# Kernel tuning notes

Hardware: AMD Instinct MI355X
Metric: run time of the kernel (lower is better)

## Reference

```python
import jax, jax.numpy as jnp
import numpy as np

N = 8192
E = 262144
H = 64


def setup_inputs() -> dict:
    key = jax.random.key(0)
    ks = jax.random.split(key, 9)
    edge_index = jax.random.randint(ks[0], (2, E), 0, N, dtype=jnp.int64)
    edge_attr = jax.random.uniform(ks[1], (E,), dtype=jnp.float32)
    node_features = jax.random.normal(ks[2], (N, N), dtype=jnp.float32)
    # GCNConv weights (glorot-ish scale) and biases
    W1 = jax.random.normal(ks[3], (N, H), dtype=jnp.float32) / np.sqrt(N)
    b1 = jnp.zeros((H,), dtype=jnp.float32)
    W2 = jax.random.normal(ks[4], (H, H), dtype=jnp.float32) / np.sqrt(H)
    b2 = jnp.zeros((H,), dtype=jnp.float32)
    fcW = jax.random.normal(ks[5], (H, N), dtype=jnp.float32) / np.sqrt(H)
    fcb = jnp.zeros((N,), dtype=jnp.float32)
    return {"edge_index": edge_index, "edge_attr": edge_attr,
            "node_features": node_features,
            "W1": W1, "b1": b1, "W2": W2, "b2": b2,
            "fcW": fcW, "fcb": fcb}


def _gcn_conv(x, W, b, src, dst, ew, n_nodes):
    # PyG GCNConv with edge weights: x' = D^{-1/2} (A + I) D^{-1/2} (x W) + b
    # src/dst/ew already include self-loops (weight 1.0).
    x = x @ W                                        # [N, out]
    deg = jax.ops.segment_sum(ew, dst, num_segments=n_nodes)  # in-degree w/ loops
    dinv = jax.lax.rsqrt(deg)                        # deg >= 1 due to self loops
    norm = dinv[src] * ew * dinv[dst]                # [E+N]
    out = jax.ops.segment_sum(x[src] * norm[:, None], dst, num_segments=n_nodes)
    return out + b


def reference(edge_index, edge_attr, node_features, W1, b1, W2, b2, fcW, fcb):
    n_nodes = node_features.shape[0]
    loops = jnp.arange(n_nodes, dtype=edge_index.dtype)
    src = jnp.concatenate([edge_index[0], loops])
    dst = jnp.concatenate([edge_index[1], loops])
    ew = jnp.concatenate([edge_attr, jnp.ones((n_nodes,), edge_attr.dtype)])
    x = jax.nn.relu(_gcn_conv(node_features, W1, b1, src, dst, ew, n_nodes))
    x = jax.nn.relu(_gcn_conv(x, W2, b2, src, dst, ew, n_nodes))
    x = x @ fcW + fcb
    return jax.nn.softmax(x, axis=-1)
```

## Files before the change

### kernel.cpp

```cpp
#include <hip/hip_runtime.h>


#define NN 8192
#define NE 262144
#define HD 64
#define KCH 1024
#define NKC 8

typedef float f32x4 __attribute__((ext_vector_type(4)));
typedef short v8s   __attribute__((ext_vector_type(8)));
typedef unsigned short ushort_t;

__device__ __forceinline__ unsigned short bf16_rne(float f){
  union { float f; unsigned u; } v; v.f = f;
  unsigned r = v.u + 0x7fffu + ((v.u >> 16) & 1u);
  return (unsigned short)(r >> 16);
}
__device__ __forceinline__ float bf16_f32(unsigned short h){
  union { unsigned u; float f; } v; v.u = ((unsigned)h) << 16;
  return v.f;
}
__device__ __forceinline__ f32x4 mfma16(v8s a, v8s b, f32x4 c){
  return __builtin_amdgcn_mfma_f32_16x16x32_bf16(a, b, c, 0, 0, 0);
}

__global__ void k_prep0(const float* __restrict__ W1, const float* __restrict__ fcW,
                        ushort_t* w1hi, ushort_t* w1lo, ushort_t* fcwp,
                        float* deg, int* cnt, int* wcnt, float* S){
  int idx = blockIdx.x*blockDim.x + threadIdx.x;
  if (idx < NN){ deg[idx]=1.0f; cnt[idx]=0; wcnt[idx]=0; S[idx]=0.0f; }
  {
    int kk = idx & 31, c = (idx>>5)&15, nt = (idx>>9)&3, kb = idx>>11;
    int k = kb*32 + kk, col = nt*16 + c;
    float w = W1[(size_t)k*HD + col];
    unsigned short hi = bf16_rne(w);
    w1hi[idx] = hi;
    w1lo[idx] = bf16_rne(w - bf16_f32(hi));
  }
  {
    int kk = idx & 31, c = (idx>>5)&15, cblk = (idx>>9)&511, kb = idx>>18;
    int k = kb*32 + kk, col = cblk*16 + c;
    fcwp[idx] = bf16_rne(fcW[(size_t)k*NN + col]);
  }
}

__global__ void k_deg_cnt(const int* ei, const float* ew, float* deg, int* cnt){
  int e = blockIdx.x*blockDim.x + threadIdx.x;
  if (e < NE){
    int d = ei[NE + e];
    atomicAdd(&deg[d], ew[e]);
    atomicAdd(&cnt[d], 1);
  }
}

__global__ void k_scan(const int* cnt, const float* deg, int* rowptr, float* dinv){
  __shared__ int part[256];
  int t = threadIdx.x;
  int loc[32]; int s = 0;
  #pragma unroll
  for (int j=0;j<32;++j){ loc[j] = cnt[t*32+j]; s += loc[j]; }
  part[t] = s; __syncthreads();
  for (int off=1; off<256; off<<=1){
    int v = (t >= off) ? part[t-off] : 0;
    __syncthreads();
    part[t] += v;
    __syncthreads();
  }
  int run = part[t] - s;
  #pragma unroll
  for (int j=0;j<32;++j){ rowptr[t*32+j] = run; run += loc[j]; }
  if (t == 255) rowptr[NN] = run;
  #pragma unroll
  for (int j=0;j<32;++j) dinv[t*32+j] = 1.0f / sqrtf(deg[t*32+j]);
}

__global__ void k_fill(const int* ei, const float* ew, const float* dinv,
                       const int* rowptr, int* wcnt, int* csr_src, float* csr_nrm){
  int e = blockIdx.x*blockDim.x + threadIdx.x;
  if (e < NE){
    int s = ei[e], d = ei[NE+e];
    int slot = rowptr[d] + atomicAdd(&wcnt[d], 1);
    csr_src[slot] = s;
    csr_nrm[slot] = dinv[s] * ew[e] * dinv[d];
  }
}

__global__ __launch_bounds__(256) void k_gemm1(const float* __restrict__ X,
                                               const ushort_t* __restrict__ w1hi,
                                               const ushort_t* __restrict__ w1lo,
                                               float* __restrict__ xw1p){
  int lane = threadIdx.x & 63, w = threadIdx.x >> 6;
  int r = lane & 15, seg = lane >> 4;
  int row = blockIdx.x*64 + w*16 + r;
  int kb0 = blockIdx.y * KCH;
  const float* xr = X + (size_t)row * NN + kb0 + seg*8;

  f32x4 z = {0.f,0.f,0.f,0.f};
  f32x4 acc[4] = {z,z,z,z};

  f32x4 p0 = *(const f32x4*)(xr);
  f32x4 p1 = *(const f32x4*)(xr + 4);

  for (int it = 0; it < KCH/32; ++it){
    f32x4 c0 = p0, c1 = p1;
    if (it < KCH/32 - 1){
      p0 = *(const f32x4*)(xr + (it+1)*32);
      p1 = *(const f32x4*)(xr + (it+1)*32 + 4);
    }
    v8s ah, al;
    #pragma unroll
    for (int j=0;j<4;++j){
      float f = c0[j]; unsigned short h = bf16_rne(f);
      ah[j] = (short)h; al[j] = (short)bf16_rne(f - bf16_f32(h));
      f = c1[j]; h = bf16_rne(f);
      ah[4+j] = (short)h; al[4+j] = (short)bf16_rne(f - bf16_f32(h));
    }
    int kbb = (kb0 >> 5) + it;
    #pragma unroll
    for (int nt=0; nt<4; ++nt){
      size_t boff = ((size_t)(kbb*4 + nt)*16 + r)*32 + seg*8;
      v8s bh = *(const v8s*)(w1hi + boff);
      v8s bl = *(const v8s*)(w1lo + boff);
      acc[nt] = mfma16(ah, bh, acc[nt]);
      acc[nt] = mfma16(ah, bl, acc[nt]);
      acc[nt] = mfma16(al, bh, acc[nt]);
    }
  }

  float* o = xw1p + (size_t)blockIdx.y*(NN*HD) + (size_t)(blockIdx.x*64 + w*16)*HD;
  #pragma unroll
  for (int nt=0; nt<4; ++nt)
    #pragma unroll
    for (int j=0;j<4;++j)
      o[(4*seg + j)*HD + nt*16 + r] = acc[nt][j];
}

__global__ __launch_bounds__(256) void k_red(const float* __restrict__ xw1p,
                                             float* __restrict__ xw1){
  int i = blockIdx.x*blockDim.x + threadIdx.x;
  f32x4 s = {0.f,0.f,0.f,0.f};
  #pragma unroll
  for (int c=0;c<NKC;++c){
    f32x4 v = *(const f32x4*)(xw1p + (size_t)c*NN*HD + (size_t)i*4);
    s[0]+=v[0]; s[1]+=v[1]; s[2]+=v[2]; s[3]+=v[3];
  }
  *(f32x4*)(xw1 + (size_t)i*4) = s;
}

__global__ __launch_bounds__(256) void k_agg1c(const float* __restrict__ xin,
                                               const float* __restrict__ b1,
                                               const float* __restrict__ W2,
                                               const float* __restrict__ dinv,
                                               const int* __restrict__ rowptr,
                                               const int* __restrict__ csr_src,
                                               const float* __restrict__ csr_nrm,
                                               float* __restrict__ x2w){
  __shared__ float W2s[64*64];
  __shared__ float rows[4][64];
  int lane = threadIdx.x & 63, w = threadIdx.x >> 6;
  for (int o = threadIdx.x; o < 64*64; o += 256) W2s[o] = W2[o];
  __syncthreads();

  int i = blockIdx.x*4 + w;
  float di = dinv[i];
  float acc = di*di * xin[(size_t)i*HD + lane];
  int e = rowptr[i], e1 = rowptr[i+1];
  for (; e + 1 < e1; e += 2){
    int s0 = csr_src[e], s1 = csr_src[e+1];
    float n0 = csr_nrm[e], n1 = csr_nrm[e+1];
    acc += n0 * xin[(size_t)s0*HD + lane];
    acc += n1 * xin[(size_t)s1*HD + lane];
  }
  if (e < e1) acc += csr_nrm[e] * xin[(size_t)csr_src[e]*HD + lane];
  float v = acc + b1[lane];
  rows[w][lane] = v > 0.f ? v : 0.f;
  __syncthreads();

  float acc2 = 0.f;
  #pragma unroll
  for (int k=0;k<64;++k) acc2 += rows[w][k] * W2s[k*64 + lane];
  x2w[(size_t)i*HD + lane] = acc2;
}

__global__ __launch_bounds__(256) void k_agg2(const float* __restrict__ xin,
                                              const float* __restrict__ b2,
                                              const float* __restrict__ dinv,
                                              const int* __restrict__ rowptr,
                                              const int* __restrict__ csr_src,
                                              const float* __restrict__ csr_nrm,
                                              ushort_t* __restrict__ x2b){
  int lane = threadIdx.x & 63, w = threadIdx.x >> 6;
  int i = blockIdx.x*4 + w;
  float di = dinv[i];
  float acc = di*di * xin[(size_t)i*HD + lane];
  int e = rowptr[i], e1 = rowptr[i+1];
  for (; e + 1 < e1; e += 2){
    int s0 = csr_src[e], s1 = csr_src[e+1];
    float n0 = csr_nrm[e], n1 = csr_nrm[e+1];
    acc += n0 * xin[(size_t)s0*HD + lane];
    acc += n1 * xin[(size_t)s1*HD + lane];
  }
  if (e < e1) acc += csr_nrm[e] * xin[(size_t)csr_src[e]*HD + lane];
  float v = acc + b2[lane];
  v = v > 0.f ? v : 0.f;
  x2b[(size_t)i*HD + lane] = bf16_rne(v);
}

__global__ __launch_bounds__(256) void k_rowsum(const ushort_t* __restrict__ x2b,
                                                const ushort_t* __restrict__ fcwp,
                                                const float* __restrict__ fcb,
                                                float* __restrict__ S){
  int lane = threadIdx.x & 63, w = threadIdx.x >> 6;
  int r = lane & 15, seg = lane >> 4;
  int row0 = blockIdx.x*128 + w*32;
  const ushort_t* xb = x2b + (size_t)(row0 + r)*HD + seg*8;
  v8s x00 = *(const v8s*)(xb);
  v8s x01 = *(const v8s*)(xb + 32);
  v8s x10 = *(const v8s*)(xb + 16*HD);
  v8s x11 = *(const v8s*)(xb + 16*HD + 32);
  float rp0 = 0.f, rp1 = 0.f;
  for (int cb=0; cb<4; ++cb){
    int colbase = blockIdx.y*256 + cb*64;
    f32x4 z = {0.f,0.f,0.f,0.f};
    f32x4 acc0[4] = {z,z,z,z}, acc1[4] = {z,z,z,z};
    #pragma unroll
    for (int nt=0; nt<4; ++nt){
      int cblk = (colbase >> 4) + nt;
      v8s bA = *(const v8s*)(fcwp + ((size_t)cblk*16 + r)*32 + seg*8);
      v8s bB = *(const v8s*)(fcwp + ((size_t)(512 + cblk)*16 + r)*32 + seg*8);
      acc0[nt] = mfma16(bA, x00, acc0[nt]);
      acc0[nt] = mfma16(bB, x01, acc0[nt]);
      acc1[nt] = mfma16(bA, x10, acc1[nt]);
      acc1[nt] = mfma16(bB, x11, acc1[nt]);
    }
    #pragma unroll
    for (int nt=0; nt<4; ++nt){
      int col = colbase + nt*16 + seg*4;
      f32x4 fb = *(const f32x4*)(fcb + col);
      #pragma unroll
      for (int j=0;j<4;++j){
        rp0 += __expf(acc0[nt][j] + fb[j]);
        rp1 += __expf(acc1[nt][j] + fb[j]);
      }
    }
  }
  rp0 += __shfl_xor(rp0, 16); rp0 += __shfl_xor(rp0, 32);
  rp1 += __shfl_xor(rp1, 16); rp1 += __shfl_xor(rp1, 32);
  if (lane < 16){
    atomicAdd(&S[row0 + lane],      rp0);
    atomicAdd(&S[row0 + 16 + lane], rp1);
  }
}

__global__ __launch_bounds__(256) void k_passB(const ushort_t* __restrict__ x2b,
                                               const ushort_t* __restrict__ fcwp,
                                               const float* __restrict__ fcb,
                                               const float* __restrict__ S,
                                               float* __restrict__ out){
  int lane = threadIdx.x & 63, w = threadIdx.x >> 6;
  int r = lane & 15, seg = lane >> 4;
  int row0 = blockIdx.x*128 + w*32;
  const ushort_t* xb = x2b + (size_t)(row0 + r)*HD + seg*8;
  v8s x00 = *(const v8s*)(xb);
  v8s x01 = *(const v8s*)(xb + 32);
  v8s x10 = *(const v8s*)(xb + 16*HD);
  v8s x11 = *(const v8s*)(xb + 16*HD + 32);
  float si0 = 1.0f / S[row0 + r];
  float si1 = 1.0f / S[row0 + 16 + r];
  float* o0 = out + (size_t)(row0 + r)*NN;
  float* o1 = out + (size_t)(row0 + 16 + r)*NN;
  for (int cb=0; cb<4; ++cb){
    int colbase = blockIdx.y*256 + cb*64;
    f32x4 z = {0.f,0.f,0.f,0.f};
    f32x4 acc0[4] = {z,z,z,z}, acc1[4] = {z,z,z,z};
    #pragma unroll
    for (int nt=0; nt<4; ++nt){
      int cblk = (colbase >> 4) + nt;
      v8s bA = *(const v8s*)(fcwp + ((size_t)cblk*16 + r)*32 + seg*8);
      v8s bB = *(const v8s*)(fcwp + ((size_t)(512 + cblk)*16 + r)*32 + seg*8);
      acc0[nt] = mfma16(bA, x00, acc0[nt]);
      acc0[nt] = mfma16(bB, x01, acc0[nt]);
      acc1[nt] = mfma16(bA, x10, acc1[nt]);
      acc1[nt] = mfma16(bB, x11, acc1[nt]);
    }
    #pragma unroll
    for (int nt=0; nt<4; ++nt){
      int col = colbase + nt*16 + seg*4;
      f32x4 fb = *(const f32x4*)(fcb + col);
      f32x4 v0, v1;
      #pragma unroll
      for (int j=0;j<4;++j){
        v0[j] = __expf(acc0[nt][j] + fb[j]) * si0;
        v1[j] = __expf(acc1[nt][j] + fb[j]) * si1;
      }
      *(f32x4*)(o0 + col) = v0;
      *(f32x4*)(o1 + col) = v1;
    }
  }
}

extern "C" void kernel_launch(void* const* d_in, const int* in_sizes, int n_in,
                              void* d_out, int out_size, void* d_ws, size_t ws_size,
                              hipStream_t stream){
  (void)in_sizes; (void)n_in; (void)out_size; (void)ws_size;
  const int*   ei  = (const int*)  d_in[0];
  const float* ew  = (const float*)d_in[1];
  const float* X   = (const float*)d_in[2];
  const float* W1  = (const float*)d_in[3];
  const float* b1  = (const float*)d_in[4];
  const float* W2  = (const float*)d_in[5];
  const float* b2  = (const float*)d_in[6];
  const float* fcW = (const float*)d_in[7];
  const float* fcb = (const float*)d_in[8];
  float* out = (float*)d_out;
  char*  ws  = (char*)d_ws;

  float*    deg     = (float*)   (ws + 0);
  float*    dinv    = (float*)   (ws + 32768);
  int*      cnt     = (int*)     (ws + 65536);
  int*      wcnt    = (int*)     (ws + 98304);
  int*      rowptr  = (int*)     (ws + 131072);
  int*      csr_src = (int*)     (ws + 167936);
  float*    csr_nrm = (float*)   (ws + 1216512);
  ushort_t* w1hi    = (ushort_t*)(ws + 2265088);
  ushort_t* w1lo    = (ushort_t*)(ws + 3313664);
  ushort_t* fcwp    = (ushort_t*)(ws + 4362240);
  float*    xw1p    = (float*)   (ws + 5410816);
  float*    xw1     = (float*)   (ws + 22188032);
  float*    x2w     = (float*)   (ws + 24285184);
  ushort_t* x2b     = (ushort_t*)(ws + 26382336);
  float*    S       = (float*)   (ws + 27430912);

  k_prep0   <<<2048, 256, 0, stream>>>(W1, fcW, w1hi, w1lo, fcwp, deg, cnt, wcnt, S);
  k_deg_cnt <<<1024, 256, 0, stream>>>(ei, ew, deg, cnt);
  k_scan    <<<1,    256, 0, stream>>>(cnt, deg, rowptr, dinv);
  k_fill    <<<1024, 256, 0, stream>>>(ei, ew, dinv, rowptr, wcnt, csr_src, csr_nrm);
  k_gemm1   <<<dim3(128, NKC), 256, 0, stream>>>(X, w1hi, w1lo, xw1p);
  k_red     <<<512,  256, 0, stream>>>(xw1p, xw1);
  k_agg1c   <<<2048, 256, 0, stream>>>(xw1, b1, W2, dinv, rowptr, csr_src, csr_nrm, x2w);
  k_agg2    <<<2048, 256, 0, stream>>>(x2w, b2, dinv, rowptr, csr_src, csr_nrm, x2b);
  k_rowsum  <<<dim3(64,32), 256, 0, stream>>>(x2b, fcwp, fcb, S);
  k_passB   <<<dim3(64,32), 256, 0, stream>>>(x2b, fcwp, fcb, S, out);
}
```

Baseline: 320.8 us.

## Register-block two row tiles per wave in GEMM1 with double-buffered prefetch

Each wave in the split-bf16 GEMM over X·W1 now computes 32 rows instead of 16, so every W1 hi/lo fragment loaded feeds twice as many MFMAs and the grid halves. A and B fragments are double-buffered two iterations ahead in registers, and the fp32-to-bf16 hi/lo split uses truncation instead of round-to-nearest-even to save ALU work. In exchange the kernel holds more registers, which launch_bounds(256,2) tries to bound, and the grid drops to 512 blocks, which may leave CUs underused. Truncation also changes the rounding of the hi/lo split slightly.

```diff
diff --git a/kernel.cpp b/kernel.cpp
--- a/kernel.cpp
+++ b/kernel.cpp
@@ -22,6 +22,14 @@
 }
 __device__ __forceinline__ f32x4 mfma16(v8s a, v8s b, f32x4 c){
   return __builtin_amdgcn_mfma_f32_16x16x32_bf16(a, b, c, 0, 0, 0);
+}
+
+__device__ __forceinline__ void split_tr(float f, short& hi, short& lo){
+  unsigned u = __float_as_uint(f);
+  hi = (short)(u >> 16);
+  float fh = __uint_as_float(u & 0xffff0000u);
+  float d = f - fh;
+  lo = (short)(__float_as_uint(d) >> 16);
 }
 
 __global__ void k_prep0(const float* __restrict__ W1, const float* __restrict__ fcW,
@@ -85,54 +93,82 @@
   }
 }
 
-__global__ __launch_bounds__(256) void k_gemm1(const float* __restrict__ X,
-                                               const ushort_t* __restrict__ w1hi,
-                                               const ushort_t* __restrict__ w1lo,
-                                               float* __restrict__ xw1p){
+__global__ __launch_bounds__(256, 2) void k_gemm1(const float* __restrict__ X,
+                                                  const ushort_t* __restrict__ w1hi,
+                                                  const ushort_t* __restrict__ w1lo,
+                                                  float* __restrict__ xw1p){
   int lane = threadIdx.x & 63, w = threadIdx.x >> 6;
   int r = lane & 15, seg = lane >> 4;
-  int row = blockIdx.x*64 + w*16 + r;
+  int row0 = blockIdx.x*128 + w*32;
   int kb0 = blockIdx.y * KCH;
-  const float* xr = X + (size_t)row * NN + kb0 + seg*8;
+  const float* xr0 = X + (size_t)(row0 + r)      * NN + kb0 + seg*8;
+  const float* xr1 = X + (size_t)(row0 + 16 + r) * NN + kb0 + seg*8;
+  const ushort_t* bhp = w1hi + (size_t)(kb0 >> 5)*2048 + r*32 + seg*8;
+  const ushort_t* blp = w1lo + (size_t)(kb0 >> 5)*2048 + r*32 + seg*8;
 
   f32x4 z = {0.f,0.f,0.f,0.f};
-  f32x4 acc[4] = {z,z,z,z};
-
-  f32x4 p0 = *(const f32x4*)(xr);
-  f32x4 p1 = *(const f32x4*)(xr + 4);
-
-  for (int it = 0; it < KCH/32; ++it){
-    f32x4 c0 = p0, c1 = p1;
-    if (it < KCH/32 - 1){
-      p0 = *(const f32x4*)(xr + (it+1)*32);
-      p1 = *(const f32x4*)(xr + (it+1)*32 + 4);
-    }
-    v8s ah, al;
+  f32x4 acc0[4] = {z,z,z,z};
+  f32x4 acc1[4] = {z,z,z,z};
+
+  f32x4 A00_0, A01_0, A10_0, A11_0;
+  f32x4 A00_1, A01_1, A10_1, A11_1;
+  v8s bh0[4], bl0[4], bh1[4], bl1[4];
+
+  A00_0 = *(const f32x4*)(xr0);        A01_0 = *(const f32x4*)(xr0 + 4);
+  A10_0 = *(const f32x4*)(xr1);        A11_0 = *(const f32x4*)(xr1 + 4);
+  A00_1 = *(const f32x4*)(xr0 + 32);   A01_1 = *(const f32x4*)(xr0 + 36);
+  A10_1 = *(const f32x4*)(xr1 + 32);   A11_1 = *(const f32x4*)(xr1 + 36);
+  #pragma unroll
+  for (int nt=0; nt<4; ++nt){
+    bh0[nt] = *(const v8s*)(bhp + nt*512);
+    bl0[nt] = *(const v8s*)(blp + nt*512);
+    bh1[nt] = *(const v8s*)(bhp + 2048 + nt*512);
+    bl1[nt] = *(const v8s*)(blp + 2048 + nt*512);
+  }
+
+  auto body = [&](int it, f32x4& A00, f32x4& A01, f32x4& A10, f32x4& A11,
+                  v8s (&bh)[4], v8s (&bl)[4]){
+    v8s ah0, al0, ah1, al1;
     #pragma unroll
     for (int j=0;j<4;++j){
-      float f = c0[j]; unsigned short h = bf16_rne(f);
-      ah[j] = (short)h; al[j] = (short)bf16_rne(f - bf16_f32(h));
-      f = c1[j]; h = bf16_rne(f);
-      ah[4+j] = (short)h; al[4+j] = (short)bf16_rne(f - bf16_f32(h));
-    }
-    int kbb = (kb0 >> 5) + it;
-    #pragma unroll
-    for (int nt=0; nt<4; ++nt){
-      size_t boff = ((size_t)(kbb*4 + nt)*16 + r)*32 + seg*8;
-      v8s bh = *(const v8s*)(w1hi + boff);
-      v8s bl = *(const v8s*)(w1lo + boff);
-      acc[nt] = mfma16(ah, bh, acc[nt]);
-      acc[nt] = mfma16(ah, bl, acc[nt]);
-      acc[nt] = mfma16(al, bh, acc[nt]);
-    }
-  }
-
-  float* o = xw1p + (size_t)blockIdx.y*(NN*HD) + (size_t)(blockIdx.x*64 + w*16)*HD;
+      short h,l;
+      split_tr(A00[j], h, l); ah0[j]   = h; al0[j]   = l;
+      split_tr(A01[j], h, l); ah0[4+j] = h; al0[4+j] = l;
+      split_tr(A10[j], h, l); ah1[j]   = h; al1[j]   = l;
+      split_tr(A11[j], h, l); ah1[4+j] = h; al1[4+j] = l;
+    }
+    int itn = (it + 2) & 31;
+    A00 = *(const f32x4*)(xr0 + itn*32);  A01 = *(const f32x4*)(xr0 + itn*32 + 4);
+    A10 = *(const f32x4*)(xr1 + itn*32);  A11 = *(const f32x4*)(xr1 + itn*32 + 4);
+    #pragma unroll
+    for (int nt=0; nt<4; ++nt){
+      acc0[nt] = mfma16(ah0, bh[nt], acc0[nt]);
+      acc0[nt] = mfma16(ah0, bl[nt], acc0[nt]);
+      acc0[nt] = mfma16(al0, bh[nt], acc0[nt]);
+      acc1[nt] = mfma16(ah1, bh[nt], acc1[nt]);
+      acc1[nt] = mfma16(ah1, bl[nt], acc1[nt]);
+      acc1[nt] = mfma16(al1, bh[nt], acc1[nt]);
+    }
+    #pragma unroll
+    for (int nt=0; nt<4; ++nt){
+      bh[nt] = *(const v8s*)(bhp + (size_t)itn*2048 + nt*512);
+      bl[nt] = *(const v8s*)(blp + (size_t)itn*2048 + nt*512);
+    }
+  };
+
+  for (int j = 0; j < 16; ++j){
+    body(2*j,     A00_0, A01_0, A10_0, A11_0, bh0, bl0);
+    body(2*j + 1, A00_1, A01_1, A10_1, A11_1, bh1, bl1);
+  }
+
+  float* o = xw1p + (size_t)blockIdx.y*(NN*HD) + (size_t)row0*HD;
   #pragma unroll
   for (int nt=0; nt<4; ++nt)
     #pragma unroll
-    for (int j=0;j<4;++j)
-      o[(4*seg + j)*HD + nt*16 + r] = acc[nt][j];
+    for (int j=0;j<4;++j){
+      o[(4*seg + j)*HD + nt*16 + r]        = acc0[nt][j];
+      o[(16 + 4*seg + j)*HD + nt*16 + r]   = acc1[nt][j];
+    }
 }
 
 __global__ __launch_bounds__(256) void k_red(const float* __restrict__ xw1p,
@@ -335,7 +371,7 @@
   k_deg_cnt <<<1024, 256, 0, stream>>>(ei, ew, deg, cnt);
   k_scan    <<<1,    256, 0, stream>>>(cnt, deg, rowptr, dinv);
   k_fill    <<<1024, 256, 0, stream>>>(ei, ew, dinv, rowptr, wcnt, csr_src, csr_nrm);
-  k_gemm1   <<<dim3(128, NKC), 256, 0, stream>>>(X, w1hi, w1lo, xw1p);
+  k_gemm1   <<<dim3(64, NKC), 256, 0, stream>>>(X, w1hi, w1lo, xw1p);
   k_red     <<<512,  256, 0, stream>>>(xw1p, xw1);
   k_agg1c   <<<2048, 256, 0, stream>>>(xw1, b1, W2, dinv, rowptr, csr_src, csr_nrm, x2w);
   k_agg2    <<<2048, 256, 0, stream>>>(x2w, b2, dinv, rowptr, csr_src, csr_nrm, x2b);
```

Result: faster. 302.6 us (-5.7%).

## Stage GEMM1 tiles through LDS with async global_load_lds double buffering

Applied to the files above, without the earlier changes.

Rewrites the first GEMM so that X and the split W1 tiles are loaded directly into double-buffered shared memory with global_load_lds, using XOR-swizzled layouts to avoid bank conflicts. W1 is stored pre-swizzled in prep to match. The fp32 to hi/lo bf16 split for the A operand now truncates instead of rounding to nearest, which saves ALU work but changes the error profile slightly. Adds a per-iteration block barrier and an occupancy hint in the launch bounds.

```diff
diff --git a/kernel.cpp b/kernel.cpp
--- a/kernel.cpp
+++ b/kernel.cpp
@@ -22,6 +22,18 @@
 }
 __device__ __forceinline__ f32x4 mfma16(v8s a, v8s b, f32x4 c){
   return __builtin_amdgcn_mfma_f32_16x16x32_bf16(a, b, c, 0, 0, 0);
+}
+__device__ __forceinline__ void split_tr(float f, short& hi, short& lo){
+  unsigned u = __float_as_uint(f);
+  hi = (short)(u >> 16);
+  float fh = __uint_as_float(u & 0xffff0000u);
+  float d = f - fh;
+  lo = (short)(__float_as_uint(d) >> 16);
+}
+__device__ __forceinline__ void gload16(const void* g, void* l){
+  __builtin_amdgcn_global_load_lds(
+      (const __attribute__((address_space(1))) unsigned int*)g,
+      (__attribute__((address_space(3))) unsigned int*)l, 16, 0, 0);
 }
 
 __global__ void k_prep0(const float* __restrict__ W1, const float* __restrict__ fcW,
@@ -34,8 +46,10 @@
     int k = kb*32 + kk, col = nt*16 + c;
     float w = W1[(size_t)k*HD + col];
     unsigned short hi = bf16_rne(w);
-    w1hi[idx] = hi;
-    w1lo[idx] = bf16_rne(w - bf16_f32(hi));
+    int chunk = idx >> 3, e = idx & 7;
+    int sidx = ((chunk ^ (c & 7)) << 3) | e;
+    w1hi[sidx] = hi;
+    w1lo[sidx] = bf16_rne(w - bf16_f32(hi));
   }
   {
     int kk = idx & 31, c = (idx>>5)&15, cblk = (idx>>9)&511, kb = idx>>18;
@@ -85,49 +99,74 @@
   }
 }
 
-__global__ __launch_bounds__(256) void k_gemm1(const float* __restrict__ X,
-                                               const ushort_t* __restrict__ w1hi,
-                                               const ushort_t* __restrict__ w1lo,
-                                               float* __restrict__ xw1p){
-  int lane = threadIdx.x & 63, w = threadIdx.x >> 6;
+__global__ __launch_bounds__(256, 4) void k_gemm1(const float* __restrict__ X,
+                                                  const ushort_t* __restrict__ w1hi,
+                                                  const ushort_t* __restrict__ w1lo,
+                                                  float* __restrict__ xw1p){
+  __shared__ __align__(16) char bufA[2][64*128];
+  __shared__ __align__(16) char bufBh[2][4096];
+  __shared__ __align__(16) char bufBl[2][4096];
+  int tid = threadIdx.x, lane = tid & 63, w = tid >> 6;
   int r = lane & 15, seg = lane >> 4;
-  int row = blockIdx.x*64 + w*16 + r;
+  int l8 = lane >> 3, l7 = lane & 7;
+  int row0 = blockIdx.x*64;
   int kb0 = blockIdx.y * KCH;
-  const float* xr = X + (size_t)row * NN + kb0 + seg*8;
+
+  const char* Xb = (const char*)X;
+  size_t asrc0 = ((size_t)(row0 + w*16 +     l8) << 15) + ((size_t)(l7 ^ l8) << 4) + ((size_t)kb0 << 2);
+  size_t asrc1 = ((size_t)(row0 + w*16 + 8 + l8) << 15) + ((size_t)(l7 ^ l8) << 4) + ((size_t)kb0 << 2);
+  const char* bhb = (const char*)w1hi + ((size_t)(kb0 >> 5) << 12) + w*1024 + lane*16;
+  const char* blb = (const char*)w1lo + ((size_t)(kb0 >> 5) << 12) + w*1024 + lane*16;
 
   f32x4 z = {0.f,0.f,0.f,0.f};
   f32x4 acc[4] = {z,z,z,z};
 
-  f32x4 p0 = *(const f32x4*)(xr);
-  f32x4 p1 = *(const f32x4*)(xr + 4);
-
-  for (int it = 0; it < KCH/32; ++it){
-    f32x4 c0 = p0, c1 = p1;
-    if (it < KCH/32 - 1){
-      p0 = *(const f32x4*)(xr + (it+1)*32);
-      p1 = *(const f32x4*)(xr + (it+1)*32 + 4);
-    }
+  int arow = (w*16 + r)*128;
+  int ac0 = ((seg*2    ) ^ (r & 7)) << 4;
+  int ac1 = ((seg*2 + 1) ^ (r & 7)) << 4;
+  int bc[4];
+  #pragma unroll
+  for (int nt=0; nt<4; ++nt)
+    bc[nt] = ((nt*64 + r*4 + seg) ^ (r & 7)) << 4;
+
+  const int NT = KCH/32;
+
+  gload16(Xb + asrc0, &bufA[0][w*2048]);
+  gload16(Xb + asrc1, &bufA[0][w*2048 + 1024]);
+  gload16(bhb, &bufBh[0][w*1024]);
+  gload16(blb, &bufBl[0][w*1024]);
+  __syncthreads();
+
+  for (int t = 0; t < NT; ++t){
+    int cur = t & 1;
+    if (t + 1 < NT){
+      size_t ka = (size_t)(t+1)*128;
+      gload16(Xb + asrc0 + ka, &bufA[cur^1][w*2048]);
+      gload16(Xb + asrc1 + ka, &bufA[cur^1][w*2048 + 1024]);
+      gload16(bhb + (size_t)(t+1)*4096, &bufBh[cur^1][w*1024]);
+      gload16(blb + (size_t)(t+1)*4096, &bufBl[cur^1][w*1024]);
+    }
+    f32x4 a0 = *(const f32x4*)(&bufA[cur][arow + ac0]);
+    f32x4 a1 = *(const f32x4*)(&bufA[cur][arow + ac1]);
     v8s ah, al;
     #pragma unroll
     for (int j=0;j<4;++j){
-      float f = c0[j]; unsigned short h = bf16_rne(f);
-      ah[j] = (short)h; al[j] = (short)bf16_rne(f - bf16_f32(h));
-      f = c1[j]; h = bf16_rne(f);
-      ah[4+j] = (short)h; al[4+j] = (short)bf16_rne(f - bf16_f32(h));
-    }
-    int kbb = (kb0 >> 5) + it;
-    #pragma unroll
-    for (int nt=0; nt<4; ++nt){
-      size_t boff = ((size_t)(kbb*4 + nt)*16 + r)*32 + seg*8;
-      v8s bh = *(const v8s*)(w1hi + boff);
-      v8s bl = *(const v8s*)(w1lo + boff);
+      short h,l;
+      split_tr(a0[j], h, l); ah[j]   = h; al[j]   = l;
+      split_tr(a1[j], h, l); ah[4+j] = h; al[4+j] = l;
+    }
+    #pragma unroll
+    for (int nt=0; nt<4; ++nt){
+      v8s bh = *(const v8s*)(&bufBh[cur][bc[nt]]);
+      v8s bl = *(const v8s*)(&bufBl[cur][bc[nt]]);
       acc[nt] = mfma16(ah, bh, acc[nt]);
       acc[nt] = mfma16(ah, bl, acc[nt]);
       acc[nt] = mfma16(al, bh, acc[nt]);
     }
-  }
-
-  float* o = xw1p + (size_t)blockIdx.y*(NN*HD) + (size_t)(blockIdx.x*64 + w*16)*HD;
+    __syncthreads();
+  }
+
+  float* o = xw1p + (size_t)blockIdx.y*(NN*HD) + (size_t)(row0 + w*16)*HD;
   #pragma unroll
   for (int nt=0; nt<4; ++nt)
     #pragma unroll
```

New measurement: 299.5 us, median of 4. 1.07x faster.

## Stage GEMM1 operands through double-buffered LDS with async global-to-LDS loads

Applied to the files above, without the earlier changes.

Rewrites the first large GEMM so that X tiles and the pre-split W1 hi/lo tiles are copied into LDS with global_load_lds, double-buffered across 128-wide K groups with XOR swizzling. This overlaps the next group's loads with the current MFMA work and lets each block share B tiles, instead of every wave reading B from global memory. It also replaces the round-to-nearest bf16 split with a cheaper truncating split. It needs 128KB of dynamic LDS at one block per CU, which reduces occupancy, and the truncation slightly changes numerics.

```diff
diff --git a/kernel.cpp b/kernel.cpp
--- a/kernel.cpp
+++ b/kernel.cpp
@@ -6,6 +6,7 @@
 #define HD 64
 #define KCH 1024
 #define NKC 8
+#define NGR 8
 
 typedef float f32x4 __attribute__((ext_vector_type(4)));
 typedef short v8s   __attribute__((ext_vector_type(8)));
@@ -22,6 +23,18 @@
 }
 __device__ __forceinline__ f32x4 mfma16(v8s a, v8s b, f32x4 c){
   return __builtin_amdgcn_mfma_f32_16x16x32_bf16(a, b, c, 0, 0, 0);
+}
+__device__ __forceinline__ void split_tr(float f, short& hi, short& lo){
+  unsigned u = __float_as_uint(f);
+  hi = (short)(u >> 16);
+  float fh = __uint_as_float(u & 0xffff0000u);
+  float d = f - fh;
+  lo = (short)(__float_as_uint(d) >> 16);
+}
+__device__ __forceinline__ void gload16(const void* g, void* l){
+  __builtin_amdgcn_global_load_lds(
+      (const __attribute__((address_space(1))) unsigned int*)g,
+      (__attribute__((address_space(3))) unsigned int*)l, 16, 0, 0);
 }
 
 __global__ void k_prep0(const float* __restrict__ W1, const float* __restrict__ fcW,
@@ -85,49 +98,90 @@
   }
 }
 
-__global__ __launch_bounds__(256) void k_gemm1(const float* __restrict__ X,
-                                               const ushort_t* __restrict__ w1hi,
-                                               const ushort_t* __restrict__ w1lo,
-                                               float* __restrict__ xw1p){
+__global__ __launch_bounds__(256, 1) void k_gemm1(const float* __restrict__ X,
+                                                  const ushort_t* __restrict__ w1hi,
+                                                  const ushort_t* __restrict__ w1lo,
+                                                  float* __restrict__ xw1p){
+  extern __shared__ __align__(16) char smem[];
+  char* bufA  = smem;
+  char* bufBh = smem + 65536;
+  char* bufBl = smem + 98304;
   int lane = threadIdx.x & 63, w = threadIdx.x >> 6;
   int r = lane & 15, seg = lane >> 4;
-  int row = blockIdx.x*64 + w*16 + r;
-  int kb0 = blockIdx.y * KCH;
-  const float* xr = X + (size_t)row * NN + kb0 + seg*8;
+  int l31 = lane & 31, lhi = lane >> 5;
+  int row0 = blockIdx.x*64, kb0 = blockIdx.y*KCH;
+
+  const char* Xb = (const char*)X;
+  size_t asrc[8];
+  #pragma unroll
+  for (int i=0;i<8;++i){
+    int row = w*16 + 2*i + lhi;
+    asrc[i] = (size_t)(row0 + row)*32768 + (size_t)kb0*4
+            + (size_t)((l31 ^ (row & 7)) * 16);
+  }
+  size_t bsrc0 = ((size_t)(kb0 >> 5))*4096 + (size_t)w*4096 + (size_t)lane*16;
 
   f32x4 z = {0.f,0.f,0.f,0.f};
   f32x4 acc[4] = {z,z,z,z};
 
-  f32x4 p0 = *(const f32x4*)(xr);
-  f32x4 p1 = *(const f32x4*)(xr + 4);
-
-  for (int it = 0; it < KCH/32; ++it){
-    f32x4 c0 = p0, c1 = p1;
-    if (it < KCH/32 - 1){
-      p0 = *(const f32x4*)(xr + (it+1)*32);
-      p1 = *(const f32x4*)(xr + (it+1)*32 + 4);
-    }
-    v8s ah, al;
+  {
+    char* aB = bufA + (w*16)*512;
+    #pragma unroll
+    for (int i=0;i<8;++i) gload16(Xb + asrc[i], aB + i*1024);
+    const char* bh = (const char*)w1hi + bsrc0;
+    const char* bl = (const char*)w1lo + bsrc0;
     #pragma unroll
     for (int j=0;j<4;++j){
-      float f = c0[j]; unsigned short h = bf16_rne(f);
-      ah[j] = (short)h; al[j] = (short)bf16_rne(f - bf16_f32(h));
-      f = c1[j]; h = bf16_rne(f);
-      ah[4+j] = (short)h; al[4+j] = (short)bf16_rne(f - bf16_f32(h));
-    }
-    int kbb = (kb0 >> 5) + it;
-    #pragma unroll
-    for (int nt=0; nt<4; ++nt){
-      size_t boff = ((size_t)(kbb*4 + nt)*16 + r)*32 + seg*8;
-      v8s bh = *(const v8s*)(w1hi + boff);
-      v8s bl = *(const v8s*)(w1lo + boff);
-      acc[nt] = mfma16(ah, bh, acc[nt]);
-      acc[nt] = mfma16(ah, bl, acc[nt]);
-      acc[nt] = mfma16(al, bh, acc[nt]);
-    }
-  }
-
-  float* o = xw1p + (size_t)blockIdx.y*(NN*HD) + (size_t)(blockIdx.x*64 + w*16)*HD;
+      gload16(bh + j*1024, bufBh + w*4096 + j*1024);
+      gload16(bl + j*1024, bufBl + w*4096 + j*1024);
+    }
+  }
+  __syncthreads();
+
+  for (int g = 0; g < NGR; ++g){
+    int cur = g & 1;
+    if (g + 1 < NGR){
+      char* aB = bufA + (cur^1)*32768 + (w*16)*512;
+      #pragma unroll
+      for (int i=0;i<8;++i) gload16(Xb + asrc[i] + (size_t)(g+1)*512, aB + i*1024);
+      const char* bh = (const char*)w1hi + bsrc0 + (size_t)(g+1)*16384;
+      const char* bl = (const char*)w1lo + bsrc0 + (size_t)(g+1)*16384;
+      char* bhB = bufBh + (cur^1)*16384 + w*4096;
+      char* blB = bufBl + (cur^1)*16384 + w*4096;
+      #pragma unroll
+      for (int j=0;j<4;++j){
+        gload16(bh + j*1024, bhB + j*1024);
+        gload16(bl + j*1024, blB + j*1024);
+      }
+    }
+    const char* aB  = bufA  + cur*32768 + (w*16 + r)*512;
+    const char* bhB = bufBh + cur*16384;
+    const char* blB = bufBl + cur*16384;
+    #pragma unroll
+    for (int tt=0; tt<4; ++tt){
+      f32x4 a0 = *(const f32x4*)(aB + (((tt*8 + seg*2    ) ^ (r & 7)) << 4));
+      f32x4 a1 = *(const f32x4*)(aB + (((tt*8 + seg*2 + 1) ^ (r & 7)) << 4));
+      v8s ah, al;
+      #pragma unroll
+      for (int j=0;j<4;++j){
+        short h,l;
+        split_tr(a0[j], h, l); ah[j]   = h; al[j]   = l;
+        split_tr(a1[j], h, l); ah[4+j] = h; al[4+j] = l;
+      }
+      #pragma unroll
+      for (int nt=0; nt<4; ++nt){
+        int fo = tt*4096 + nt*1024 + r*64 + seg*16;
+        v8s bh = *(const v8s*)(bhB + fo);
+        v8s bl = *(const v8s*)(blB + fo);
+        acc[nt] = mfma16(ah, bh, acc[nt]);
+        acc[nt] = mfma16(ah, bl, acc[nt]);
+        acc[nt] = mfma16(al, bh, acc[nt]);
+      }
+    }
+    __syncthreads();
+  }
+
+  float* o = xw1p + (size_t)blockIdx.y*(NN*HD) + (size_t)(row0 + w*16)*HD;
   #pragma unroll
   for (int nt=0; nt<4; ++nt)
     #pragma unroll
@@ -331,11 +385,18 @@
   ushort_t* x2b     = (ushort_t*)(ws + 26382336);
   float*    S       = (float*)   (ws + 27430912);
 
+  static bool attr_set = false;
+  if (!attr_set){
+    hipFuncSetAttribute((const void*)k_gemm1,
+                        hipFuncAttributeMaxDynamicSharedMemorySize, 131072);
+    attr_set = true;
+  }
+
   k_prep0   <<<2048, 256, 0, stream>>>(W1, fcW, w1hi, w1lo, fcwp, deg, cnt, wcnt, S);
   k_deg_cnt <<<1024, 256, 0, stream>>>(ei, ew, deg, cnt);
   k_scan    <<<1,    256, 0, stream>>>(cnt, deg, rowptr, dinv);
   k_fill    <<<1024, 256, 0, stream>>>(ei, ew, dinv, rowptr, wcnt, csr_src, csr_nrm);
-  k_gemm1   <<<dim3(128, NKC), 256, 0, stream>>>(X, w1hi, w1lo, xw1p);
+  k_gemm1   <<<dim3(128, NKC), 256, 131072, stream>>>(X, w1hi, w1lo, xw1p);
   k_red     <<<512,  256, 0, stream>>>(xw1p, xw1);
   k_agg1c   <<<2048, 256, 0, stream>>>(xw1, b1, W2, dinv, rowptr, csr_src, csr_nrm, x2w);
   k_agg2    <<<2048, 256, 0, stream>>>(x2w, b2, dinv, rowptr, csr_src, csr_nrm, x2b);
```

Result: faster. 305.2 us (-4.9%).
